# Kernel optimization log

Measured on AMD Instinct MI355X. Metric: run time of the kernel, lower is better.

## Reference

```python
import jax, jax.numpy as jnp
import numpy as np

ALPHA = 0.2  # LeakyReLU negative slope
NEG_INF = -9e15


def _gat_layer(Wh, adj, a, concat):
    """One GraphAttentionLayer given pre-projected Wh [B,N,F].
    Algebraic split of the concat attention: e[b,i,j] = lrelu(Wh[i]@a1 + Wh[j]@a2),
    identical math to matmul(cat(Wh_i, Wh_j), a)."""
    F_ = Wh.shape[-1]
    f1 = Wh @ a[:F_, 0]   # [B,N]
    f2 = Wh @ a[F_:, 0]   # [B,N]
    e = jax.nn.leaky_relu(f1[:, :, None] + f2[:, None, :], negative_slope=ALPHA)  # [B,N,N]
    e = jnp.where(adj > 0, e, NEG_INF)
    att = jax.nn.softmax(e, axis=-1)            # dropout omitted (eval mode)
    h_prime = jnp.einsum('bij,bjf->bif', att, Wh)
    return jax.nn.elu(h_prime) if concat else h_prime


def setup_inputs() -> dict:
    key = jax.random.key(0)
    ks = jax.random.split(key, 9)
    B, N, Fin, H, nH, Fout = 4, 2048, 512, 128, 4, 256
    x = jax.random.normal(ks[0], (B, N, Fin), dtype=jnp.float32)
    adj = jax.random.randint(ks[1], (B, N, N), 0, 2, dtype=jnp.int32)
    mask = jnp.ones((B, N), dtype=jnp.float32)
    s = 0.05
    W_heads = jax.random.normal(ks[2], (nH, Fin, H), dtype=jnp.float32) * s
    a_heads = jax.random.normal(ks[3], (nH, 2 * H, 1), dtype=jnp.float32) * s
    W_out = jax.random.normal(ks[4], (nH * H, Fout), dtype=jnp.float32) * s
    a_out = jax.random.normal(ks[5], (2 * Fout, 1), dtype=jnp.float32) * s
    W_pool = jax.random.normal(ks[6], (Fout, Fout), dtype=jnp.float32) * s
    b_pool = jax.random.normal(ks[7], (Fout,), dtype=jnp.float32) * s
    return {"x": x, "adj": adj, "mask": mask, "W_heads": W_heads, "a_heads": a_heads,
            "W_out": W_out, "a_out": a_out, "W_pool": W_pool, "b_pool": b_pool}


def reference(x, adj, mask, W_heads, a_heads, W_out, a_out, W_pool, b_pool):
    # multi-head GAT layer, heads concatenated (dropout = identity in eval)
    heads = [_gat_layer(x @ W_heads[h], adj, a_heads[h], concat=True)
             for h in range(W_heads.shape[0])]
    xcat = jnp.concatenate(heads, axis=-1)                 # [B,N,nH*H]
    x_out = _gat_layer(xcat @ W_out, adj, a_out, concat=False)  # [B,N,Fout]
    x_out = x_out * mask[:, :, None]
    pooled = x_out.sum(axis=1) / (mask.sum(axis=1, keepdims=True) + 1e-10)
    graph_embedding = jax.nn.relu(pooled @ W_pool + b_pool)
    return graph_embedding, x_out
```

## Files before the change

kernel.cpp:

```cpp
#include <hip/hip_runtime.h>

typedef unsigned short u16;
typedef __attribute__((ext_vector_type(8))) short s8v;
typedef __attribute__((ext_vector_type(8))) unsigned short us8;
typedef __attribute__((ext_vector_type(4))) float f4v;

#define L2E 1.4426950408889634f

typedef __attribute__((address_space(1))) void gvoid_t;
typedef __attribute__((address_space(3))) void lvoid_t;

__device__ __forceinline__ u16 f2bf(float f) {
  unsigned u = __builtin_bit_cast(unsigned, f);
  return (u16)((u + 0x7FFFu + ((u >> 16) & 1u)) >> 16);
}
__device__ __forceinline__ float bf2f(u16 h) {
  return __builtin_bit_cast(float, ((unsigned)h) << 16);
}
__device__ __forceinline__ f4v mfma16(s8v a, s8v b, f4v c) {
  return __builtin_amdgcn_mfma_f32_16x16x32_bf16(a, b, c, 0, 0, 0);
}
__device__ __forceinline__ float exp2fast(float x) {
#if __has_builtin(__builtin_amdgcn_exp2f)
  return __builtin_amdgcn_exp2f(x);
#else
  return exp2f(x);
#endif
}
__device__ __forceinline__ void stage16(const u16* g, u16* lds_arr, int slot) {
#if __has_builtin(__builtin_amdgcn_global_load_lds)
  __builtin_amdgcn_global_load_lds((gvoid_t*)(g),
      (lvoid_t*)(lds_arr + (size_t)(slot & ~63) * 8), 16, 0, 0);
#else
  *(us8*)(lds_arr + (size_t)slot * 8) = *(const us8*)g;
#endif
}

__global__ __launch_bounds__(256) void prep_x(const float* __restrict__ x,
                                              u16* __restrict__ xb) {
  int i = (blockIdx.x * 256 + threadIdx.x) * 8;
  float4 v0 = *(const float4*)(x + i);
  float4 v1 = *(const float4*)(x + i + 4);
  us8 o;
  o[0] = f2bf(v0.x); o[1] = f2bf(v0.y); o[2] = f2bf(v0.z); o[3] = f2bf(v0.w);
  o[4] = f2bf(v1.x); o[5] = f2bf(v1.y); o[6] = f2bf(v1.z); o[7] = f2bf(v1.w);
  *(us8*)(xb + i) = o;
}

__global__ __launch_bounds__(256) void prep_wall(const float* __restrict__ W,
                                                 u16* __restrict__ Wt) {
  int idx = blockIdx.x * 256 + threadIdx.x;
  int h = idx >> 16, k = (idx >> 7) & 511, f = idx & 127;
  Wt[(size_t)(h * 128 + f) * 512 + k] = f2bf(W[idx]);
}
__global__ __launch_bounds__(256) void prep_wout(const float* __restrict__ W,
                                                 u16* __restrict__ Wt) {
  int idx = blockIdx.x * 256 + threadIdx.x;
  int k = idx >> 8, c = idx & 255;
  Wt[(size_t)c * 512 + k] = f2bf(W[idx]);
}
__global__ __launch_bounds__(256) void prep_adj(const int* __restrict__ adj,
                                                unsigned* __restrict__ adjw) {
  int chunk = blockIdx.x * 4 + (threadIdx.x >> 6);
  int l = threadIdx.x & 63;
  int v = adj[(size_t)chunk * 64 + l];
  unsigned long long m = __ballot(v != 0);
  if (l == 0) {
    ((uint2*)adjw)[chunk] = make_uint2((unsigned)m, (unsigned)(m >> 32));
  }
}

__global__ __launch_bounds__(256) void gemm_bf16(const u16* __restrict__ A,
                                                 const u16* __restrict__ Bt,
                                                 u16* __restrict__ Ct, int CO) {
  const int K = 512, N = 2048;
  int m0 = blockIdx.x * 128;
  int n0 = blockIdx.y * 128;
  int t = threadIdx.x;
  int w = t >> 6, l = t & 63, lr = l & 15, lq = l >> 4;
  int wr = w >> 1, wc = w & 1;
  __shared__ u16 As[2][128 * 32];
  __shared__ u16 Bs[2][128 * 32];
  f4v zero4 = {0.f, 0.f, 0.f, 0.f};
  f4v acc[4][4];
#pragma unroll
  for (int i = 0; i < 4; ++i)
#pragma unroll
    for (int j = 0; j < 4; ++j) acc[i][j] = zero4;

  auto stage = [&](int buf, int kt) {
    int k0 = kt * 32;
    int row = t >> 2, ch = t & 3;
    stage16(A + (size_t)(m0 + row) * K + k0 + ch * 8, As[buf], t);
    stage16(Bt + (size_t)(n0 + row) * K + k0 + ch * 8, Bs[buf], t);
    int s2 = t + 256;
    row = s2 >> 2; ch = s2 & 3;
    stage16(A + (size_t)(m0 + row) * K + k0 + ch * 8, As[buf], s2);
    stage16(Bt + (size_t)(n0 + row) * K + k0 + ch * 8, Bs[buf], s2);
  };
  stage(0, 0);
  for (int kt = 0; kt < 16; ++kt) {
    __syncthreads();
    if (kt < 15) stage((kt + 1) & 1, kt + 1);
    const u16* as = As[kt & 1];
    const u16* bs = Bs[kt & 1];
    s8v af[4], bfr[4];
#pragma unroll
    for (int rf = 0; rf < 4; ++rf)
      af[rf] = *(const s8v*)&as[(wr * 64 + rf * 16 + lr) * 32 + lq * 8];
#pragma unroll
    for (int nf = 0; nf < 4; ++nf)
      bfr[nf] = *(const s8v*)&bs[(wc * 64 + nf * 16 + lr) * 32 + lq * 8];
#pragma unroll
    for (int rf = 0; rf < 4; ++rf)
#pragma unroll
      for (int nf = 0; nf < 4; ++nf)
        acc[rf][nf] = mfma16(af[rf], bfr[nf], acc[rf][nf]);
  }
  int bidx = m0 >> 11;
  int nr0 = m0 & 2047;
#pragma unroll
  for (int rf = 0; rf < 4; ++rf) {
#pragma unroll
    for (int nf = 0; nf < 4; ++nf) {
      int col = n0 + wc * 64 + nf * 16 + lr;
      int nr = nr0 + wr * 64 + rf * 16 + lq * 4;
      f4v a = acc[rf][nf];
      ushort4 v = make_ushort4(f2bf(a[0]), f2bf(a[1]), f2bf(a[2]), f2bf(a[3]));
      *(ushort4*)&Ct[((size_t)bidx * CO + col) * N + nr] = v;
    }
  }
}

__global__ __launch_bounds__(256) void fkern(const u16* __restrict__ Wht,
                                             const float* __restrict__ a,
                                             float* __restrict__ f1L,
                                             float* __restrict__ f2L, int COLS,
                                             int F) {
  const int N = 2048;
  int h = blockIdx.z, b = blockIdx.y;
  int nl = threadIdx.x & 63, fc = threadIdx.x >> 6;
  int n = blockIdx.x * 64 + nl;
  int F4 = F >> 2;
  const u16* colp = Wht + ((size_t)(b * COLS + h * F + fc * F4)) * N + n;
  const float* ah = a + h * 2 * F + fc * F4;
  float a1 = 0.f, a2 = 0.f;
  for (int c = 0; c < F4; ++c) {
    float v = bf2f(colp[(size_t)c * N]);
    a1 = fmaf(v, ah[c], a1);
    a2 = fmaf(v, ah[F + c], a2);
  }
  __shared__ float r1[4][64], r2[4][64];
  r1[fc][nl] = a1;
  r2[fc][nl] = a2;
  __syncthreads();
  if (fc == 0) {
    float s1 = r1[0][nl] + r1[1][nl] + r1[2][nl] + r1[3][nl];
    float s2 = r2[0][nl] + r2[1][nl] + r2[2][nl] + r2[3][nl];
    f1L[(size_t)(h * 4 + b) * N + n] = s1 * L2E;
    f2L[(size_t)(h * 4 + b) * N + n] = s2 * L2E;
  }
}

__global__ __launch_bounds__(256) void fmax_kern(const float* __restrict__ f2L,
                                                 float* __restrict__ f2m) {
  int row = blockIdx.x;
  const float* p = f2L + (size_t)row * 2048;
  int t = threadIdx.x;
  float v = -__builtin_inff();
  for (int k = 0; k < 8; ++k) v = fmaxf(v, p[t + k * 256]);
#pragma unroll
  for (int d = 1; d < 64; d <<= 1) v = fmaxf(v, __shfl_xor(v, d));
  __shared__ float wm[4];
  if ((t & 63) == 0) wm[t >> 6] = v;
  __syncthreads();
  if (t == 0) f2m[row] = fmaxf(fmaxf(wm[0], wm[1]), fmaxf(wm[2], wm[3]));
}

template <int CT, int NCH, int RF, bool ELU>
__global__ __launch_bounds__(256, 2) void attn_kernel(
    const u16* __restrict__ Wht, const float* __restrict__ f1L,
    const float* __restrict__ f2L, const float* __restrict__ f2max,
    const unsigned* __restrict__ adjw, const float* __restrict__ mask,
    void* __restrict__ outp) {
  const int N = 2048;
  constexpr int ROWS = RF * 32;
  constexpr int NT = 2048 / ROWS;
  constexpr int FHD = (CT == 512) ? 1 : 0;
  int kb = blockIdx.x;
  int x = kb & 7, g = kb >> 3;
  int p = x + 8 * (g / NT);
  int it = g % NT;
  int b = p / NCH, ch = p % NCH;
  int i0 = it * ROWS, col0 = ch * 128;
  int fh = FHD ? ch : 0;
  int t = threadIdx.x;
  int w = t >> 6, l = t & 63, lr = l & 15, lq = l >> 4;
  int wr = w >> 1, wc = w & 1;

  __shared__ u16 Vs[2][128 * 64];
  __shared__ unsigned adjs[ROWS * 65];
  __shared__ float f2s[2048];

  const float* f1p = f1L + (size_t)(fh * 4 + b) * N + i0;
  const float* f2p = f2L + (size_t)(fh * 4 + b) * N;
  float f2m = f2max[fh * 4 + b];
  float c1[RF], c2[RF];
#pragma unroll
  for (int rf = 0; rf < RF; ++rf) {
    float f1v = f1p[wr * RF * 16 + rf * 16 + lr];
    float su = f1v + f2m;
    float M = fmaxf(su, 0.2f * su);
    c1[rf] = f1v - M;
    c2[rf] = 0.2f * f1v - M;
  }
  const u16* vbase = Wht + (size_t)(b * CT + col0) * 2048;

  for (int i = t; i < ROWS * 64; i += 256) {
    int row = i >> 6, wd = i & 63;
    adjs[row * 65 + wd] = adjw[(size_t)(b * N + i0 + row) * 64 + wd];
  }
  for (int i = t; i < 2048; i += 256) f2s[i] = f2p[i];

  auto stage = [&](int buf, int kt) {
    int k0 = kt * 64;
#pragma unroll
    for (int j2 = 0; j2 < 4; ++j2) {
      int s = j2 * 256 + t;
      int c = s >> 3, q = s & 7;
      stage16(vbase + (size_t)c * 2048 + k0 + q * 8, Vs[buf], s);
    }
  };
  stage(0, 0);

  f4v zero4 = {0.f, 0.f, 0.f, 0.f};
  f4v acc[RF][4];
#pragma unroll
  for (int rf = 0; rf < RF; ++rf)
#pragma unroll
    for (int j = 0; j < 4; ++j) acc[rf][j] = zero4;
  float s_[RF];
#pragma unroll
  for (int rf = 0; rf < RF; ++rf) s_[rf] = 0.f;

  for (int kt = 0; kt < 32; ++kt) {
    __syncthreads();
    if (kt < 31) stage((kt + 1) & 1, kt + 1);
    const u16* vs = Vs[kt & 1];
#pragma unroll
    for (int kk = 0; kk < 2; ++kk) {
      int jt = kt * 2 + kk;
      s8v vf[4];
#pragma unroll
      for (int nf = 0; nf < 4; ++nf)
        vf[nf] = *(const s8v*)&vs[(wc * 64 + nf * 16 + lr) * 64 + kk * 32 +
                                  lq * 8];
      float4 fa = *(const float4*)&f2s[jt * 32 + lq * 8];
      float4 fb = *(const float4*)&f2s[jt * 32 + lq * 8 + 4];
      float f2c[8] = {fa.x, fa.y, fa.z, fa.w, fb.x, fb.y, fb.z, fb.w};
      s8v pa[RF];
#pragma unroll
      for (int rf = 0; rf < RF; ++rf) {
        unsigned aw = adjs[(wr * RF * 16 + rf * 16 + lr) * 65 + jt];
        union { s8v v; unsigned u[4]; } pk;
#pragma unroll
        for (int ep = 0; ep < 4; ++ep) {
          float t1 = c1[rf] + f2c[2 * ep];
          float t2 = fmaf(0.2f, f2c[2 * ep], c2[rf]);
          float p0 = exp2fast(fmaxf(t1, t2));
          p0 = ((aw >> (lq * 8 + 2 * ep)) & 1u) ? p0 : 0.f;
          s_[rf] += p0;
          float t3 = c1[rf] + f2c[2 * ep + 1];
          float t4 = fmaf(0.2f, f2c[2 * ep + 1], c2[rf]);
          float p1 = exp2fast(fmaxf(t3, t4));
          p1 = ((aw >> (lq * 8 + 2 * ep + 1)) & 1u) ? p1 : 0.f;
          s_[rf] += p1;
          asm("v_cvt_pk_bf16_f32 %0, %1, %2"
              : "=v"(pk.u[ep]) : "v"(p0), "v"(p1));
        }
        pa[rf] = pk.v;
      }
#pragma unroll
      for (int nf = 0; nf < 4; ++nf)
#pragma unroll
        for (int rf = 0; rf < RF; ++rf)
          acc[rf][nf] = mfma16(pa[rf], vf[nf], acc[rf][nf]);
    }
  }
#pragma unroll
  for (int rf = 0; rf < RF; ++rf) {
    s_[rf] += __shfl_xor(s_[rf], 16);
    s_[rf] += __shfl_xor(s_[rf], 32);
  }
#pragma unroll
  for (int rf = 0; rf < RF; ++rf) {
    float inv = 1.f / fmaxf(s_[rf], 1e-30f);
    f4v i4;
#pragma unroll
    for (int r = 0; r < 4; ++r) i4[r] = __shfl(inv, lq * 4 + r);
    int rowb = i0 + wr * RF * 16 + rf * 16 + lq * 4;
#pragma unroll
    for (int nf = 0; nf < 4; ++nf) {
      int col = col0 + wc * 64 + nf * 16 + lr;
#pragma unroll
      for (int r = 0; r < 4; ++r) {
        float v = acc[rf][nf][r] * i4[r];
        size_t ob = (size_t)(b * N + rowb + r) * CT + col;
        if constexpr (ELU) {
          v = v > 0.f ? v : exp2fast(v * L2E) - 1.f;
          ((u16*)outp)[ob] = f2bf(v);
        } else {
          ((float*)outp)[ob] = v * mask[b * N + rowb + r];
        }
      }
    }
  }
}

__global__ __launch_bounds__(256) void pool1(const float* __restrict__ xout,
                                             const float* __restrict__ mask,
                                             float* __restrict__ pool,
                                             float* __restrict__ den) {
  int b = blockIdx.x >> 6, s = blockIdx.x & 63;
  int c = threadIdx.x;
  int n0 = s * 32;
  float acc = 0.f;
  for (int r = 0; r < 32; ++r)
    acc += xout[((size_t)(b * 2048 + n0 + r)) * 256 + c];
  atomicAdd(&pool[b * 256 + c], acc);
  if (c == 0) {
    float ms = 0.f;
    for (int r = 0; r < 32; ++r) ms += mask[b * 2048 + n0 + r];
    atomicAdd(&den[b], ms);
  }
}
__global__ __launch_bounds__(256) void pool2(const float* __restrict__ pool,
                                             const float* __restrict__ den,
                                             const float* __restrict__ Wp,
                                             const float* __restrict__ bp,
                                             float* __restrict__ out) {
  int b = blockIdx.x, f = threadIdx.x;
  __shared__ float pv[256];
  float inv = 1.f / (den[b] + 1e-10f);
  pv[f] = pool[b * 256 + f] * inv;
  __syncthreads();
  float acc = bp[f];
  for (int c = 0; c < 256; ++c) acc = fmaf(pv[c], Wp[c * 256 + f], acc);
  out[b * 256 + f] = fmaxf(acc, 0.f);
}

extern "C" void kernel_launch(void* const* d_in, const int* in_sizes, int n_in,
                              void* d_out, int out_size, void* d_ws,
                              size_t ws_size, hipStream_t stream) {
  (void)in_sizes; (void)n_in; (void)out_size; (void)ws_size;
  const float* x = (const float*)d_in[0];
  const int* adj = (const int*)d_in[1];
  const float* mask = (const float*)d_in[2];
  const float* Whds = (const float*)d_in[3];
  const float* ahds = (const float*)d_in[4];
  const float* Wout = (const float*)d_in[5];
  const float* aout = (const float*)d_in[6];
  const float* Wpool = (const float*)d_in[7];
  const float* bpool = (const float*)d_in[8];
  float* out = (float*)d_out;

  char* ws = (char*)d_ws;
  size_t off = 0;
  auto take = [&](size_t n) {
    char* p = ws + off;
    off += (n + 255) & ~(size_t)255;
    return p;
  };
  u16* xb = (u16*)take(8192ull * 512 * 2);
  u16* Wta = (u16*)take(512ull * 512 * 2);
  u16* Wto = (u16*)take(256ull * 512 * 2);
  unsigned* adjw = (unsigned*)take(4ull * 2048 * 64 * 4);
  u16* Wht = (u16*)take(4ull * 512 * 2048 * 2);
  float* f1a = (float*)take(4ull * 4 * 2048 * 4);
  float* f2a = (float*)take(4ull * 4 * 2048 * 4);
  u16* xcat = (u16*)take(8192ull * 512 * 2);
  u16* Wh2t = (u16*)take(4ull * 256 * 2048 * 2);
  float* f1b = (float*)take(4ull * 2048 * 4);
  float* f2b = (float*)take(4ull * 2048 * 4);
  float* f2ma = (float*)take(16 * 4);
  float* f2mb = (float*)take(4 * 4);
  float* pool = (float*)take(1024 * 4);
  float* den = (float*)take(256);

  prep_x<<<2048, 256, 0, stream>>>(x, xb);
  prep_wall<<<1024, 256, 0, stream>>>(Whds, Wta);
  prep_wout<<<512, 256, 0, stream>>>(Wout, Wto);
  prep_adj<<<65536, 256, 0, stream>>>(adj, adjw);
  gemm_bf16<<<dim3(64, 4), 256, 0, stream>>>(xb, Wta, Wht, 512);
  fkern<<<dim3(32, 4, 4), 256, 0, stream>>>(Wht, ahds, f1a, f2a, 512, 128);
  fmax_kern<<<16, 256, 0, stream>>>(f2a, f2ma);
  attn_kernel<512, 4, 2, true><<<512, 256, 0, stream>>>(Wht, f1a, f2a, f2ma,
                                                        adjw, nullptr, xcat);
  gemm_bf16<<<dim3(64, 2), 256, 0, stream>>>(xcat, Wto, Wh2t, 256);
  fkern<<<dim3(32, 4, 1), 256, 0, stream>>>(Wh2t, aout, f1b, f2b, 256, 256);
  fmax_kern<<<4, 256, 0, stream>>>(f2b, f2mb);
  attn_kernel<256, 2, 1, false><<<512, 256, 0, stream>>>(Wh2t, f1b, f2b, f2mb,
                                                         adjw, mask,
                                                         out + 1024);
  hipMemsetAsync(pool, 0, 4096 + 256, stream);
  pool1<<<256, 256, 0, stream>>>(out + 1024, mask, pool, den);
  pool2<<<4, 256, 0, stream>>>(pool, den, Wpool, bpool, out);
}
```

Baseline: 202.1 us.

## Remap attention waves to full-width column tiles to avoid duplicate softmax exps

Each wave now owns 16 query rows across all 128 output columns, instead of a 2x2 wave grid where two waves recomputed the same exp/mask probabilities for shared rows. This removes the duplicated exponent and adjacency work per tile. In exchange, each wave reads twice as many V fragments from LDS and holds 8 accumulators. The second attention launch also moves to 64-row tiles, which halves its grid to 256 blocks.

```diff
diff --git a/kernel.cpp b/kernel.cpp
--- a/kernel.cpp
+++ b/kernel.cpp
@@ -177,14 +177,15 @@
   if (t == 0) f2m[row] = fmaxf(fmaxf(wm[0], wm[1]), fmaxf(wm[2], wm[3]));
 }
 
-template <int CT, int NCH, int RF, bool ELU>
+template <int CT, bool ELU>
 __global__ __launch_bounds__(256, 2) void attn_kernel(
     const u16* __restrict__ Wht, const float* __restrict__ f1L,
     const float* __restrict__ f2L, const float* __restrict__ f2max,
     const unsigned* __restrict__ adjw, const float* __restrict__ mask,
     void* __restrict__ outp) {
   const int N = 2048;
-  constexpr int ROWS = RF * 32;
+  constexpr int NCH = CT / 128;
+  constexpr int ROWS = 64;
   constexpr int NT = 2048 / ROWS;
   constexpr int FHD = (CT == 512) ? 1 : 0;
   int kb = blockIdx.x;
@@ -196,7 +197,6 @@
   int fh = FHD ? ch : 0;
   int t = threadIdx.x;
   int w = t >> 6, l = t & 63, lr = l & 15, lq = l >> 4;
-  int wr = w >> 1, wc = w & 1;
 
   __shared__ u16 Vs[2][128 * 64];
   __shared__ unsigned adjs[ROWS * 65];
@@ -205,15 +205,11 @@
   const float* f1p = f1L + (size_t)(fh * 4 + b) * N + i0;
   const float* f2p = f2L + (size_t)(fh * 4 + b) * N;
   float f2m = f2max[fh * 4 + b];
-  float c1[RF], c2[RF];
-#pragma unroll
-  for (int rf = 0; rf < RF; ++rf) {
-    float f1v = f1p[wr * RF * 16 + rf * 16 + lr];
-    float su = f1v + f2m;
-    float M = fmaxf(su, 0.2f * su);
-    c1[rf] = f1v - M;
-    c2[rf] = 0.2f * f1v - M;
-  }
+  float f1v = f1p[w * 16 + lr];
+  float su = f1v + f2m;
+  float M = fmaxf(su, 0.2f * su);
+  float c1 = f1v - M;
+  float c2 = 0.2f * f1v - M;
   const u16* vbase = Wht + (size_t)(b * CT + col0) * 2048;
 
   for (int i = t; i < ROWS * 64; i += 256) {
@@ -234,14 +230,10 @@
   stage(0, 0);
 
   f4v zero4 = {0.f, 0.f, 0.f, 0.f};
-  f4v acc[RF][4];
-#pragma unroll
-  for (int rf = 0; rf < RF; ++rf)
-#pragma unroll
-    for (int j = 0; j < 4; ++j) acc[rf][j] = zero4;
-  float s_[RF];
-#pragma unroll
-  for (int rf = 0; rf < RF; ++rf) s_[rf] = 0.f;
+  f4v acc[8];
+#pragma unroll
+  for (int j = 0; j < 8; ++j) acc[j] = zero4;
+  float s_ = 0.f;
 
   for (int kt = 0; kt < 32; ++kt) {
     __syncthreads();
@@ -250,68 +242,55 @@
 #pragma unroll
     for (int kk = 0; kk < 2; ++kk) {
       int jt = kt * 2 + kk;
-      s8v vf[4];
-#pragma unroll
-      for (int nf = 0; nf < 4; ++nf)
-        vf[nf] = *(const s8v*)&vs[(wc * 64 + nf * 16 + lr) * 64 + kk * 32 +
-                                  lq * 8];
+      s8v vf[8];
+#pragma unroll
+      for (int nf = 0; nf < 8; ++nf)
+        vf[nf] = *(const s8v*)&vs[(nf * 16 + lr) * 64 + kk * 32 + lq * 8];
       float4 fa = *(const float4*)&f2s[jt * 32 + lq * 8];
       float4 fb = *(const float4*)&f2s[jt * 32 + lq * 8 + 4];
       float f2c[8] = {fa.x, fa.y, fa.z, fa.w, fb.x, fb.y, fb.z, fb.w};
-      s8v pa[RF];
-#pragma unroll
-      for (int rf = 0; rf < RF; ++rf) {
-        unsigned aw = adjs[(wr * RF * 16 + rf * 16 + lr) * 65 + jt];
-        union { s8v v; unsigned u[4]; } pk;
-#pragma unroll
-        for (int ep = 0; ep < 4; ++ep) {
-          float t1 = c1[rf] + f2c[2 * ep];
-          float t2 = fmaf(0.2f, f2c[2 * ep], c2[rf]);
-          float p0 = exp2fast(fmaxf(t1, t2));
-          p0 = ((aw >> (lq * 8 + 2 * ep)) & 1u) ? p0 : 0.f;
-          s_[rf] += p0;
-          float t3 = c1[rf] + f2c[2 * ep + 1];
-          float t4 = fmaf(0.2f, f2c[2 * ep + 1], c2[rf]);
-          float p1 = exp2fast(fmaxf(t3, t4));
-          p1 = ((aw >> (lq * 8 + 2 * ep + 1)) & 1u) ? p1 : 0.f;
-          s_[rf] += p1;
-          asm("v_cvt_pk_bf16_f32 %0, %1, %2"
-              : "=v"(pk.u[ep]) : "v"(p0), "v"(p1));
-        }
-        pa[rf] = pk.v;
+      unsigned aw = adjs[(w * 16 + lr) * 65 + jt];
+      union { s8v v; unsigned u[4]; } pk;
+#pragma unroll
+      for (int ep = 0; ep < 4; ++ep) {
+        float t1 = c1 + f2c[2 * ep];
+        float t2 = fmaf(0.2f, f2c[2 * ep], c2);
+        float p0 = exp2fast(fmaxf(t1, t2));
+        p0 = ((aw >> (lq * 8 + 2 * ep)) & 1u) ? p0 : 0.f;
+        s_ += p0;
+        float t3 = c1 + f2c[2 * ep + 1];
+        float t4 = fmaf(0.2f, f2c[2 * ep + 1], c2);
+        float p1 = exp2fast(fmaxf(t3, t4));
+        p1 = ((aw >> (lq * 8 + 2 * ep + 1)) & 1u) ? p1 : 0.f;
+        s_ += p1;
+        asm("v_cvt_pk_bf16_f32 %0, %1, %2"
+            : "=v"(pk.u[ep]) : "v"(p0), "v"(p1));
       }
-#pragma unroll
-      for (int nf = 0; nf < 4; ++nf)
-#pragma unroll
-        for (int rf = 0; rf < RF; ++rf)
-          acc[rf][nf] = mfma16(pa[rf], vf[nf], acc[rf][nf]);
+      s8v pa = pk.v;
+#pragma unroll
+      for (int nf = 0; nf < 8; ++nf)
+        acc[nf] = mfma16(pa, vf[nf], acc[nf]);
     }
   }
-#pragma unroll
-  for (int rf = 0; rf < RF; ++rf) {
-    s_[rf] += __shfl_xor(s_[rf], 16);
-    s_[rf] += __shfl_xor(s_[rf], 32);
-  }
-#pragma unroll
-  for (int rf = 0; rf < RF; ++rf) {
-    float inv = 1.f / fmaxf(s_[rf], 1e-30f);
-    f4v i4;
-#pragma unroll
-    for (int r = 0; r < 4; ++r) i4[r] = __shfl(inv, lq * 4 + r);
-    int rowb = i0 + wr * RF * 16 + rf * 16 + lq * 4;
-#pragma unroll
-    for (int nf = 0; nf < 4; ++nf) {
-      int col = col0 + wc * 64 + nf * 16 + lr;
-#pragma unroll
-      for (int r = 0; r < 4; ++r) {
-        float v = acc[rf][nf][r] * i4[r];
-        size_t ob = (size_t)(b * N + rowb + r) * CT + col;
-        if constexpr (ELU) {
-          v = v > 0.f ? v : exp2fast(v * L2E) - 1.f;
-          ((u16*)outp)[ob] = f2bf(v);
-        } else {
-          ((float*)outp)[ob] = v * mask[b * N + rowb + r];
-        }
+  s_ += __shfl_xor(s_, 16);
+  s_ += __shfl_xor(s_, 32);
+  float inv = 1.f / fmaxf(s_, 1e-30f);
+  f4v i4;
+#pragma unroll
+  for (int r = 0; r < 4; ++r) i4[r] = __shfl(inv, lq * 4 + r);
+  int rowb = i0 + w * 16 + lq * 4;
+#pragma unroll
+  for (int nf = 0; nf < 8; ++nf) {
+    int col = col0 + nf * 16 + lr;
+#pragma unroll
+    for (int r = 0; r < 4; ++r) {
+      float v = acc[nf][r] * i4[r];
+      size_t ob = (size_t)(b * N + rowb + r) * CT + col;
+      if constexpr (ELU) {
+        v = v > 0.f ? v : exp2fast(v * L2E) - 1.f;
+        ((u16*)outp)[ob] = f2bf(v);
+      } else {
+        ((float*)outp)[ob] = v * mask[b * N + rowb + r];
       }
     }
   }
@@ -394,14 +373,13 @@
   gemm_bf16<<<dim3(64, 4), 256, 0, stream>>>(xb, Wta, Wht, 512);
   fkern<<<dim3(32, 4, 4), 256, 0, stream>>>(Wht, ahds, f1a, f2a, 512, 128);
   fmax_kern<<<16, 256, 0, stream>>>(f2a, f2ma);
-  attn_kernel<512, 4, 2, true><<<512, 256, 0, stream>>>(Wht, f1a, f2a, f2ma,
-                                                        adjw, nullptr, xcat);
+  attn_kernel<512, true><<<512, 256, 0, stream>>>(Wht, f1a, f2a, f2ma,
+                                                  adjw, nullptr, xcat);
   gemm_bf16<<<dim3(64, 2), 256, 0, stream>>>(xcat, Wto, Wh2t, 256);
   fkern<<<dim3(32, 4, 1), 256, 0, stream>>>(Wh2t, aout, f1b, f2b, 256, 256);
   fmax_kern<<<4, 256, 0, stream>>>(f2b, f2mb);
-  attn_kernel<256, 2, 1, false><<<512, 256, 0, stream>>>(Wh2t, f1b, f2b, f2mb,
-                                                         adjw, mask,
-                                                         out + 1024);
+  attn_kernel<256, false><<<256, 256, 0, stream>>>(Wh2t, f1b, f2b, f2mb,
+                                                   adjw, mask, out + 1024);
   hipMemsetAsync(pool, 0, 4096 + 256, stream);
   pool1<<<256, 256, 0, stream>>>(out + 1024, mask, pool, den);
   pool2<<<4, 256, 0, stream>>>(pool, den, Wpool, bpool, out);
```

Result: faster. 196.4 us (-2.8%).
